# Kernel optimization log

Hardware: AMD Instinct MI355X
Metric: run time of the kernel (lower is better)

Reference implementation:

```python
import jax, jax.numpy as jnp
import numpy as np

DIM = 2048
HEAD = 256
SEQ = 4096

def setup_inputs() -> dict:
    key = jax.random.key(0)
    ks = jax.random.split(key, 7)
    s = 1.0 / np.sqrt(DIM)
    return {
        "marketStateBatch": jax.random.normal(ks[0], (SEQ, DIM), dtype=jnp.float32),
        "Wq": jax.random.uniform(ks[1], (HEAD, DIM), jnp.float32, -s, s),
        "bq": jax.random.uniform(ks[2], (HEAD,), jnp.float32, -s, s),
        "Wk": jax.random.uniform(ks[3], (HEAD, DIM), jnp.float32, -s, s),
        "bk": jax.random.uniform(ks[4], (HEAD,), jnp.float32, -s, s),
        "Wv": jax.random.uniform(ks[5], (HEAD, DIM), jnp.float32, -s, s),
        "bv": jax.random.uniform(ks[6], (HEAD,), jnp.float32, -s, s),
    }

def reference(marketStateBatch, Wq, bq, Wk, bk, Wv, bv):
    x = marketStateBatch  # [S, D]
    q = x @ Wq.T + bq     # [S, H]
    k = x @ Wk.T + bk     # [S, H]
    v = x @ Wv.T + bv     # [S, H]
    # NOTE: original scales by sqrt(dimensionSize), the INPUT dim, not head dim.
    scores = (q @ k.T) * (1.0 / np.sqrt(DIM))  # [S, S]
    S = x.shape[0]
    causal = jnp.tril(jnp.ones((S, S), dtype=bool))
    scores = jnp.where(causal, scores, -jnp.inf)
    attn = jax.nn.softmax(scores, axis=-1)
    # torch.nan_to_num(attn, 0.0): rows are never all -inf here (diag kept),
    # but replicate the op faithfully.
    attn = jnp.nan_to_num(attn, nan=0.0)
    return attn @ v  # [S, H]
```

## Files before the change

### kernel.cpp

```cpp
#include <hip/hip_runtime.h>
#include <stdint.h>

#define SEQ 4096
#define DIMK 2048
#define HD 256

typedef __attribute__((ext_vector_type(8))) short bf16x8;
typedef __attribute__((ext_vector_type(4))) short u16x4;
typedef __attribute__((ext_vector_type(4))) float f32x4;
typedef __attribute__((ext_vector_type(16))) float f32x16;
typedef unsigned short u16;
typedef unsigned int u32;

#define BAR() asm volatile("s_barrier" ::: "memory")
#define VMCNT(n) asm volatile("s_waitcnt vmcnt(" #n ")" ::: "memory")

__device__ __forceinline__ u16 f2bf(float f) {
    u32 u = __float_as_uint(f);
    u += 0x7FFFu + ((u >> 16) & 1u);
    return (u16)(u >> 16);
}

__device__ __forceinline__ float bf2f(u16 h) {
    u32 u = ((u32)h) << 16;
    return __uint_as_float(u);
}

__device__ __forceinline__ bf16x8 pack8(f32x4 a0, f32x4 a1) {
    bf16x8 v8;
    v8[0]=(short)f2bf(a0[0]); v8[1]=(short)f2bf(a0[1]);
    v8[2]=(short)f2bf(a0[2]); v8[3]=(short)f2bf(a0[3]);
    v8[4]=(short)f2bf(a1[0]); v8[5]=(short)f2bf(a1[1]);
    v8[6]=(short)f2bf(a1[2]); v8[7]=(short)f2bf(a1[3]);
    return v8;
}

__device__ __forceinline__ void gl16(const void* g, void* l) {
    __builtin_amdgcn_global_load_lds(
        (const __attribute__((address_space(1))) void*)g,
        (__attribute__((address_space(3))) void*)l, 16, 0, 0);
}

__device__ __forceinline__ u32 cvtpk(float lo, float hi) {
    u32 d;
    asm("v_cvt_pk_bf16_f32 %0, %1, %2" : "=v"(d) : "v"(lo), "v"(hi));
    return d;
}

__device__ __forceinline__ void plswap(u32& x, u32& y) {
#if __has_builtin(__builtin_amdgcn_permlane32_swap)
    typedef int i32x2 __attribute__((ext_vector_type(2)));
    i32x2 r = __builtin_amdgcn_permlane32_swap((int)x, (int)y, false, false);
    x = (u32)r[0]; y = (u32)r[1];
#else
    asm("v_permlane32_swap_b32 %0, %1" : "+v"(x), "+v"(y));
#endif
}

__global__ __launch_bounds__(256) void cvt_all2(
    const float* __restrict__ x, const float* __restrict__ Wq,
    const float* __restrict__ Wk, const float* __restrict__ Wv,
    u16* __restrict__ xb_sw, u16* __restrict__ wb_sw)
{
    const int y = blockIdx.y;
    int i = blockIdx.x * 256 + threadIdx.x;
    int stride = gridDim.x * 256;
    if (y == 0) {
        for (; i < SEQ*DIMK/8; i += stride) {
            int row = i >> 8, c8 = i & 255;
            f32x4 a0 = *(const f32x4*)(x + (size_t)row*DIMK + c8*8);
            f32x4 a1 = *(const f32x4*)(x + (size_t)row*DIMK + c8*8 + 4);
            int mt = row >> 6, rl = row & 63, kt = c8 >> 3, sl = c8 & 7;
            size_t dst = ((size_t)(mt*32 + kt))*4096 + rl*64 + ((sl ^ (rl&7))*8);
            *(bf16x8*)(xb_sw + dst) = pack8(a0, a1);
        }
    } else {
        const float* W = (y==1) ? Wq : (y==2) ? Wk : Wv;
        for (; i < HD*DIMK/8; i += stride) {
            int row = i >> 8, c8 = i & 255;
            f32x4 a0 = *(const f32x4*)(W + (size_t)row*DIMK + c8*8);
            f32x4 a1 = *(const f32x4*)(W + (size_t)row*DIMK + c8*8 + 4);
            int gr = (y-1)*256 + row;
            int nt = gr >> 7, rl = gr & 127, kt = c8 >> 3, sl = c8 & 7;
            size_t dst = ((size_t)(nt*32 + kt))*8192 + rl*64 + ((sl ^ (rl&7))*8);
            *(bf16x8*)(wb_sw + dst) = pack8(a0, a1);
        }
    }
}

__global__ __launch_bounds__(256, 2) void qkv_gemm3(
    const u16* __restrict__ xb_sw, const u16* __restrict__ wb_sw,
    const float* __restrict__ bq, const float* __restrict__ bk,
    const float* __restrict__ bv,
    u16* __restrict__ qb, u16* __restrict__ kb_t, u16* __restrict__ vt_t)
{
    __shared__ char Ab[2][16384];
    __shared__ char Bb[2][16384];

    const int tid = threadIdx.x;
    const int L = tid & 63;
    const int w = tid >> 6;
    const int l31 = L & 31, h = L >> 5;
    const int wr = w >> 1, wc = w & 1;
    const int mt2 = blockIdx.x;
    const int y   = blockIdx.y;
    const int z   = y >> 1;
    const float* bias = (z==0) ? bq : (z==1) ? bk : bv;

    const u16* a0 = xb_sw + ((size_t)((mt2*2 + (w>>1))*32))*4096 + (w&1)*2048 + L*8;
    const u16* b0 = wb_sw + ((size_t)(y*32))*8192 + w*2048 + L*8;

    auto stage = [&](int kt, int b) {
        const u16* ag = a0 + (size_t)kt*4096;
        const u16* bg = b0 + (size_t)kt*8192;
        char* al = Ab[b] + w*4096;
        char* bl = Bb[b] + w*4096;
        #pragma unroll
        for (int i = 0; i < 4; ++i) gl16(ag + i*512, al + i*1024);
        #pragma unroll
        for (int i = 0; i < 4; ++i) gl16(bg + i*512, bl + i*1024);
    };

    stage(0, 0);
    stage(1, 1);

    f32x16 acc[2][2];
    #pragma unroll
    for (int m = 0; m < 2; ++m)
        #pragma unroll
        for (int n = 0; n < 2; ++n)
            #pragma unroll
            for (int e = 0; e < 16; ++e) acc[m][n][e] = 0.f;

    for (int kt = 0; kt < 32; ++kt) {
        if (kt < 31) { VMCNT(8); } else { VMCNT(0); }
        BAR();
        const char* A = Ab[kt & 1];
        const char* B = Bb[kt & 1];
        __builtin_amdgcn_s_setprio(1);
        #pragma unroll
        for (int c = 0; c < 4; ++c) {
            const int sl = 2*c + h;
            bf16x8 af[2], bfr[2];
            #pragma unroll
            for (int m = 0; m < 2; ++m) {
                int row = wr*64 + m*32 + l31;
                af[m] = *(const bf16x8*)(A + (row>>6)*8192 + (row&63)*128
                                           + ((sl ^ (row&7)) << 4));
            }
            #pragma unroll
            for (int n = 0; n < 2; ++n) {
                int brow = wc*64 + n*32 + l31;
                bfr[n] = *(const bf16x8*)(B + brow*128 + ((sl ^ (brow&7)) << 4));
            }
            #pragma unroll
            for (int m = 0; m < 2; ++m)
                #pragma unroll
                for (int n = 0; n < 2; ++n)
                    acc[m][n] = __builtin_amdgcn_mfma_f32_32x32x16_bf16(
                        af[m], bfr[n], acc[m][n], 0, 0, 0);
        }
        __builtin_amdgcn_s_setprio(0);
        BAR();
        if (kt + 2 < 32) stage(kt + 2, kt & 1);
    }

    const int m0 = mt2*128;
    const float qs = 0.03187936f;
    #pragma unroll
    for (int n = 0; n < 2; ++n) {
        const int hc = ((y&1)*128 + wc*64 + n*32 + l31) & 255;
        const float bcol = bias[hc];
        #pragma unroll
        for (int m = 0; m < 2; ++m) {
            const int rbase = m0 + wr*64 + m*32;
            if (z == 0) {
                #pragma unroll
                for (int e = 0; e < 16; ++e) {
                    int grow = rbase + (e&3) + 8*(e>>2) + 4*h;
                    qb[(size_t)grow*HD + hc] = f2bf((acc[m][n][e] + bcol) * qs);
                }
            } else if (z == 1) {
                #pragma unroll
                for (int e = 0; e < 16; ++e) {
                    int grow = rbase + (e&3) + 8*(e>>2) + 4*h;
                    int t = grow >> 5, rl = grow & 31;
                    kb_t[(size_t)t*8192 + rl*256 + (((hc>>3) ^ (rl&7))*8) + (hc&7)]
                        = f2bf(acc[m][n][e] + bcol);
                }
            } else {
                const int t = rbase >> 5;
                #pragma unroll
                for (int e4 = 0; e4 < 4; ++e4) {
                    int kl0 = 8*e4 + 4*h;
                    u16x4 pk;
                    #pragma unroll
                    for (int j = 0; j < 4; ++j)
                        pk[j] = (short)f2bf(acc[m][n][e4*4 + j] + bcol);
                    *(u16x4*)(vt_t + (size_t)t*8192 + hc*32 +
                              ((e4 ^ (hc&3) ^ ((hc>>2)&3))*8) + (kl0&7)) = pk;
                }
            }
        }
    }
}

__global__ __launch_bounds__(256, 2) void attn_part6(
    const u16* __restrict__ qb, const u16* __restrict__ kb_t,
    const u16* __restrict__ vt_t,
    u16* __restrict__ po, float* __restrict__ pm, float* __restrict__ pl,
    int C)
{
    __shared__ char Kb[2][16384];
    __shared__ char Vb[2][16384];

    const int pid = blockIdx.x;
    int Q = 0, a0 = 0;
    for (int k = 0; k < 32; ++k) {
        int nsk = (4*k + 4 + C - 1) / C;
        if (pid < a0 + nsk) { Q = k; break; }
        a0 += nsk;
    }
    const int s  = pid - a0;
    const int nt = 4*Q + 4;
    const int t0 = s*C;
    const int t1 = min(t0 + C, nt);

    const int tid = threadIdx.x;
    const int L = tid & 63;
    const int w = tid >> 6;
    const int l31 = L & 31;
    const int h   = L >> 5;
    const int qg  = Q*128 + w*32 + l31;
    const int vsw = (l31 & 3) ^ ((l31 >> 2) & 3);
    const int kx  = l31 & 7;

    auto stage = [&](int t, int b) {
        const u16* kg = kb_t + (size_t)t*8192 + w*2048 + L*8;
        const u16* vg = vt_t + (size_t)t*8192 + w*2048 + L*8;
        char* kl = Kb[b] + w*4096;
        char* vl = Vb[b] + w*4096;
        #pragma unroll
        for (int i = 0; i < 4; ++i) gl16(kg + i*512, kl + i*1024);
        #pragma unroll
        for (int i = 0; i < 4; ++i) gl16(vg + i*512, vl + i*1024);
    };

    stage(t0, t0 & 1);
    if (t0 + 1 < t1) stage(t0 + 1, (t0 + 1) & 1);
    else             stage(t0,     (t0 + 1) & 1);

    bf16x8 qf[16];
    {
        const u16* qp = qb + (size_t)qg*HD + h*8;
        #pragma unroll
        for (int c = 0; c < 16; ++c) qf[c] = *(const bf16x8*)(qp + c*16);
    }

    f32x16 o[8];
    #pragma unroll
    for (int ht = 0; ht < 8; ++ht)
        #pragma unroll
        for (int e = 0; e < 16; ++e) o[ht][e] = 0.f;
    float mrun = -1e30f, lrun = 0.f;

    for (int t = t0; t < t1; ++t) {
        if (t + 1 < t1) { VMCNT(8); } else { VMCNT(0); }
        BAR();
        const char* K = Kb[t & 1];
        const char* V = Vb[t & 1];

        #define LDK(c) (*(const bf16x8*)(K + l31*512 + (((2*(c) + h) ^ kx) << 4)))
        f32x16 sv;
        #pragma unroll
        for (int e = 0; e < 16; ++e) sv[e] = 0.f;
        __builtin_amdgcn_s_setprio(1);
        {
            bf16x8 ka = LDK(0), kb_ = LDK(1), kc = LDK(2), kd = LDK(3);
            sv = __builtin_amdgcn_mfma_f32_32x32x16_bf16(ka,  qf[0],  sv, 0,0,0); ka  = LDK(4);
            sv = __builtin_amdgcn_mfma_f32_32x32x16_bf16(kb_, qf[1],  sv, 0,0,0); kb_ = LDK(5);
            sv = __builtin_amdgcn_mfma_f32_32x32x16_bf16(kc,  qf[2],  sv, 0,0,0); kc  = LDK(6);
            sv = __builtin_amdgcn_mfma_f32_32x32x16_bf16(kd,  qf[3],  sv, 0,0,0); kd  = LDK(7);
            sv = __builtin_amdgcn_mfma_f32_32x32x16_bf16(ka,  qf[4],  sv, 0,0,0); ka  = LDK(8);
            sv = __builtin_amdgcn_mfma_f32_32x32x16_bf16(kb_, qf[5],  sv, 0,0,0); kb_ = LDK(9);
            sv = __builtin_amdgcn_mfma_f32_32x32x16_bf16(kc,  qf[6],  sv, 0,0,0); kc  = LDK(10);
            sv = __builtin_amdgcn_mfma_f32_32x32x16_bf16(kd,  qf[7],  sv, 0,0,0); kd  = LDK(11);
            sv = __builtin_amdgcn_mfma_f32_32x32x16_bf16(ka,  qf[8],  sv, 0,0,0); ka  = LDK(12);
            sv = __builtin_amdgcn_mfma_f32_32x32x16_bf16(kb_, qf[9],  sv, 0,0,0); kb_ = LDK(13);
            sv = __builtin_amdgcn_mfma_f32_32x32x16_bf16(kc,  qf[10], sv, 0,0,0); kc  = LDK(14);
            sv = __builtin_amdgcn_mfma_f32_32x32x16_bf16(kd,  qf[11], sv, 0,0,0); kd  = LDK(15);
            sv = __builtin_amdgcn_mfma_f32_32x32x16_bf16(ka,  qf[12], sv, 0,0,0);
            sv = __builtin_amdgcn_mfma_f32_32x32x16_bf16(kb_, qf[13], sv, 0,0,0);
            sv = __builtin_amdgcn_mfma_f32_32x32x16_bf16(kc,  qf[14], sv, 0,0,0);
            sv = __builtin_amdgcn_mfma_f32_32x32x16_bf16(kd,  qf[15], sv, 0,0,0);
        }
        #undef LDK
        __builtin_amdgcn_s_setprio(0);

        if (t*32 + 31 > Q*128 + w*32) {
            #pragma unroll
            for (int e = 0; e < 16; ++e) {
                int kvr = (e & 3) + 8*(e >> 2) + 4*h;
                if (t*32 + kvr > qg) sv[e] = -__builtin_inff();
            }
        }

        float m0_ = fmaxf(fmaxf(sv[0],sv[1]),  fmaxf(sv[2],sv[3]));
        float m1_ = fmaxf(fmaxf(sv[4],sv[5]),  fmaxf(sv[6],sv[7]));
        float m2_ = fmaxf(fmaxf(sv[8],sv[9]),  fmaxf(sv[10],sv[11]));
        float m3_ = fmaxf(fmaxf(sv[12],sv[13]),fmaxf(sv[14],sv[15]));
        float mx = fmaxf(fmaxf(m0_,m1_), fmaxf(m2_,m3_));
        mx = fmaxf(mx, __shfl_xor(mx, 32));
        if (__any(mx > mrun + 8.0f)) {
            float mnew  = fmaxf(mrun, mx);
            float alpha = exp2f(mrun - mnew);
            lrun *= alpha;
            #pragma unroll
            for (int ht = 0; ht < 8; ++ht) o[ht] *= alpha;
            mrun = mnew;
        }
        #pragma unroll
        for (int e = 0; e < 16; ++e) sv[e] = exp2f(sv[e] - mrun);
        float r0 = ((sv[0]+sv[1])+(sv[2]+sv[3])) + ((sv[4]+sv[5])+(sv[6]+sv[7]));
        float r1 = ((sv[8]+sv[9])+(sv[10]+sv[11])) + ((sv[12]+sv[13])+(sv[14]+sv[15]));
        float rs = r0 + r1;
        rs += __shfl_xor(rs, 32);
        lrun += rs;

        union { u32 wd[4]; bf16x8 v8; } up0, up1;
        {
            u32 A = cvtpk(sv[0],  sv[1]),  B = cvtpk(sv[2],  sv[3]);
            u32 Cc= cvtpk(sv[4],  sv[5]),  D = cvtpk(sv[6],  sv[7]);
            plswap(A, Cc); plswap(B, D);
            up0.wd[0]=A; up0.wd[1]=B; up0.wd[2]=Cc; up0.wd[3]=D;
            u32 A1 = cvtpk(sv[8],  sv[9]),  B1 = cvtpk(sv[10], sv[11]);
            u32 C1 = cvtpk(sv[12], sv[13]), D1 = cvtpk(sv[14], sv[15]);
            plswap(A1, C1); plswap(B1, D1);
            up1.wd[0]=A1; up1.wd[1]=B1; up1.wd[2]=C1; up1.wd[3]=D1;
        }
        bf16x8 pa0 = up0.v8, pa1 = up1.v8;

        __builtin_amdgcn_s_setprio(1);
        #pragma unroll
        for (int ht = 0; ht < 8; ++ht) {
            const char* vrow = V + (ht*32 + l31)*64;
            bf16x8 vf0 = *(const bf16x8*)(vrow + (((h)     ^ vsw) << 4));
            bf16x8 vf1 = *(const bf16x8*)(vrow + (((2 + h) ^ vsw) << 4));
            o[ht] = __builtin_amdgcn_mfma_f32_32x32x16_bf16(vf0, pa0, o[ht], 0, 0, 0);
            o[ht] = __builtin_amdgcn_mfma_f32_32x32x16_bf16(vf1, pa1, o[ht], 0, 0, 0);
        }
        __builtin_amdgcn_s_setprio(0);

        BAR();
        stage(min(t + 2, t1 - 1), t & 1);
    }

    VMCNT(0);

    if (h == 0) {
        pm[(size_t)pid*128 + w*32 + l31] = mrun;
        pl[(size_t)pid*128 + w*32 + l31] = lrun;
    }
    u16* op = po + ((size_t)pid*128 + w*32 + l31) * 256;
    #pragma unroll
    for (int ht = 0; ht < 8; ++ht)
        #pragma unroll
        for (int j = 0; j < 8; ++j) {
            u32 pk = (u32)f2bf(o[ht][2*j]) | ((u32)f2bf(o[ht][2*j+1]) << 16);
            int hdb = ht*32 + (j & 1)*2 + (j >> 1)*8 + 4*h;
            *(u32*)(op + hdb) = pk;
        }
}

__global__ __launch_bounds__(256) void attn_combine5(
    const u16* __restrict__ po, const float* __restrict__ pm,
    const float* __restrict__ pl, float* __restrict__ out, int C)
{
    const int tid = threadIdx.x;
    const int row = blockIdx.x * 16 + (tid >> 4);
    const int cg  = tid & 15;
    const int Q   = row >> 7, rr = row & 127;
    const int nt  = 4*Q + 4;
    const int ns  = (nt + C - 1) / C;
    int pid0 = 0;
    for (int k = 0; k < Q; ++k) pid0 += (4*k + 4 + C - 1) / C;

    float M = -1e30f;
    for (int s = 0; s < ns; ++s)
        M = fmaxf(M, pm[(size_t)(pid0+s)*128 + rr]);

    float lt = 0.f;
    f32x4 acc[4];
    f32x4 zero = {0.f,0.f,0.f,0.f};
    #pragma unroll
    for (int v = 0; v < 4; ++v) acc[v] = zero;

    for (int s = 0; s < ns; ++s) {
        float ms  = pm[(size_t)(pid0+s)*128 + rr];
        float wgt = exp2f(ms - M);
        lt += wgt * pl[(size_t)(pid0+s)*128 + rr];
        const u16* p = po + ((size_t)(pid0+s)*128 + rr)*256 + cg*16;
        #pragma unroll
        for (int v = 0; v < 4; ++v) {
            u16x4 pv = *(const u16x4*)(p + v*4);
            #pragma unroll
            for (int e = 0; e < 4; ++e)
                acc[v][e] += wgt * bf2f((u16)pv[e]);
        }
    }
    float inv = 1.f / lt;
    f32x4* op = (f32x4*)(out + (size_t)row*256 + cg*16);
    #pragma unroll
    for (int v = 0; v < 4; ++v) op[v] = acc[v] * inv;
}

extern "C" void kernel_launch(void* const* d_in, const int* in_sizes, int n_in,
                              void* d_out, int out_size, void* d_ws, size_t ws_size,
                              hipStream_t stream) {
    const float* x  = (const float*)d_in[0];
    const float* Wq = (const float*)d_in[1];
    const float* bq = (const float*)d_in[2];
    const float* Wk = (const float*)d_in[3];
    const float* bk = (const float*)d_in[4];
    const float* Wv = (const float*)d_in[5];
    const float* bv = (const float*)d_in[6];
    float* out = (float*)d_out;

    const size_t xb_bytes  = (size_t)SEQ * DIMK * 2;
    const size_t wb_bytes  = (size_t)768 * DIMK * 2;
    const size_t qkv_bytes = (size_t)SEQ * HD * 2;
    const size_t base = xb_bytes + wb_bytes + 3*qkv_bytes;

    int C = 64;
    size_t npid = 0;
    const int cand[4] = {5, 8, 16, 64};
    for (int ci = 0; ci < 4; ++ci) {
        int c = cand[ci];
        size_t np = 0;
        for (int k = 0; k < 32; ++k) np += (size_t)(4*k + 4 + c - 1) / c;
        size_t need = base + np * ((size_t)128*256*2 + 2*128*4);
        if (need <= ws_size) { C = c; npid = np; break; }
        if (ci == 3) { C = c; npid = np; }
    }

    char* p = (char*)d_ws;
    u16* xb_sw = (u16*)p; p += xb_bytes;
    u16* wb_sw = (u16*)p; p += wb_bytes;
    u16* qbuf  = (u16*)p; p += qkv_bytes;
    u16* kb_t  = (u16*)p; p += qkv_bytes;
    u16* vt_t  = (u16*)p; p += qkv_bytes;
    u16* po    = (u16*)p; p += npid * 128 * 256 * 2;
    float* pm  = (float*)p; p += npid * 128 * 4;
    float* pl  = (float*)p; p += npid * 128 * 4;

    cvt_all2<<<dim3(512, 4), 256, 0, stream>>>(x, Wq, Wk, Wv, xb_sw, wb_sw);

    qkv_gemm3<<<dim3(SEQ/128, 6), 256, 0, stream>>>(
        xb_sw, wb_sw, bq, bk, bv, qbuf, kb_t, vt_t);

    attn_part6<<<(int)npid, 256, 0, stream>>>(
        qbuf, kb_t, vt_t, po, pm, pl, C);

    attn_combine5<<<SEQ/16, 256, 0, stream>>>(po, pm, pl, out, C);
}
```

Before: 93.06 us.

## Halve QKV GEMM N-tile to 64 columns and double grid for occupancy

After: 88.56 us. 1.05x faster.

```diff
diff --git a/kernel.cpp b/kernel.cpp
--- a/kernel.cpp
+++ b/kernel.cpp
@@ -88,14 +88,14 @@
     }
 }
 
-__global__ __launch_bounds__(256, 2) void qkv_gemm3(
+__global__ __launch_bounds__(256, 3) void qkv_gemm4(
     const u16* __restrict__ xb_sw, const u16* __restrict__ wb_sw,
     const float* __restrict__ bq, const float* __restrict__ bk,
     const float* __restrict__ bv,
     u16* __restrict__ qb, u16* __restrict__ kb_t, u16* __restrict__ vt_t)
 {
     __shared__ char Ab[2][16384];
-    __shared__ char Bb[2][16384];
+    __shared__ char Bb[2][8192];
 
     const int tid = threadIdx.x;
     const int L = tid & 63;
@@ -104,36 +104,34 @@
     const int wr = w >> 1, wc = w & 1;
     const int mt2 = blockIdx.x;
     const int y   = blockIdx.y;
-    const int z   = y >> 1;
+    const int z   = y >> 2;
     const float* bias = (z==0) ? bq : (z==1) ? bk : bv;
 
     const u16* a0 = xb_sw + ((size_t)((mt2*2 + (w>>1))*32))*4096 + (w&1)*2048 + L*8;
-    const u16* b0 = wb_sw + ((size_t)(y*32))*8192 + w*2048 + L*8;
+    const u16* b0 = wb_sw + ((size_t)((y>>1)*32))*8192 + (y&1)*4096 + w*1024 + L*8;
 
     auto stage = [&](int kt, int b) {
         const u16* ag = a0 + (size_t)kt*4096;
         const u16* bg = b0 + (size_t)kt*8192;
         char* al = Ab[b] + w*4096;
-        char* bl = Bb[b] + w*4096;
+        char* bl = Bb[b] + w*2048;
         #pragma unroll
         for (int i = 0; i < 4; ++i) gl16(ag + i*512, al + i*1024);
-        #pragma unroll
-        for (int i = 0; i < 4; ++i) gl16(bg + i*512, bl + i*1024);
+        gl16(bg,       bl);
+        gl16(bg + 512, bl + 1024);
     };
 
     stage(0, 0);
     stage(1, 1);
 
-    f32x16 acc[2][2];
+    f32x16 acc[2];
     #pragma unroll
     for (int m = 0; m < 2; ++m)
         #pragma unroll
-        for (int n = 0; n < 2; ++n)
-            #pragma unroll
-            for (int e = 0; e < 16; ++e) acc[m][n][e] = 0.f;
+        for (int e = 0; e < 16; ++e) acc[m][e] = 0.f;
 
     for (int kt = 0; kt < 32; ++kt) {
-        if (kt < 31) { VMCNT(8); } else { VMCNT(0); }
+        if (kt < 31) { VMCNT(6); } else { VMCNT(0); }
         BAR();
         const char* A = Ab[kt & 1];
         const char* B = Bb[kt & 1];
@@ -141,24 +139,18 @@
         #pragma unroll
         for (int c = 0; c < 4; ++c) {
             const int sl = 2*c + h;
-            bf16x8 af[2], bfr[2];
+            const int brow = wc*32 + l31;
+            bf16x8 bfr = *(const bf16x8*)(B + brow*128 + ((sl ^ (brow&7)) << 4));
+            bf16x8 af[2];
             #pragma unroll
             for (int m = 0; m < 2; ++m) {
-                int row = wr*64 + m*32 + l31;
-                af[m] = *(const bf16x8*)(A + (row>>6)*8192 + (row&63)*128
-                                           + ((sl ^ (row&7)) << 4));
+                int rlo = m*32 + l31;
+                af[m] = *(const bf16x8*)(A + wr*8192 + rlo*128 + ((sl ^ (rlo&7)) << 4));
             }
             #pragma unroll
-            for (int n = 0; n < 2; ++n) {
-                int brow = wc*64 + n*32 + l31;
-                bfr[n] = *(const bf16x8*)(B + brow*128 + ((sl ^ (brow&7)) << 4));
-            }
-            #pragma unroll
             for (int m = 0; m < 2; ++m)
-                #pragma unroll
-                for (int n = 0; n < 2; ++n)
-                    acc[m][n] = __builtin_amdgcn_mfma_f32_32x32x16_bf16(
-                        af[m], bfr[n], acc[m][n], 0, 0, 0);
+                acc[m] = __builtin_amdgcn_mfma_f32_32x32x16_bf16(
+                    af[m], bfr, acc[m], 0, 0, 0);
         }
         __builtin_amdgcn_s_setprio(0);
         BAR();
@@ -167,39 +159,36 @@
 
     const int m0 = mt2*128;
     const float qs = 0.03187936f;
-    #pragma unroll
-    for (int n = 0; n < 2; ++n) {
-        const int hc = ((y&1)*128 + wc*64 + n*32 + l31) & 255;
-        const float bcol = bias[hc];
-        #pragma unroll
-        for (int m = 0; m < 2; ++m) {
-            const int rbase = m0 + wr*64 + m*32;
-            if (z == 0) {
+    const int hc = (y & 3)*64 + wc*32 + l31;
+    const float bcol = bias[hc];
+    #pragma unroll
+    for (int m = 0; m < 2; ++m) {
+        const int rbase = m0 + wr*64 + m*32;
+        if (z == 0) {
+            #pragma unroll
+            for (int e = 0; e < 16; ++e) {
+                int grow = rbase + (e&3) + 8*(e>>2) + 4*h;
+                qb[(size_t)grow*HD + hc] = f2bf((acc[m][e] + bcol) * qs);
+            }
+        } else if (z == 1) {
+            #pragma unroll
+            for (int e = 0; e < 16; ++e) {
+                int grow = rbase + (e&3) + 8*(e>>2) + 4*h;
+                int t = grow >> 5, rl = grow & 31;
+                kb_t[(size_t)t*8192 + rl*256 + (((hc>>3) ^ (rl&7))*8) + (hc&7)]
+                    = f2bf(acc[m][e] + bcol);
+            }
+        } else {
+            const int t = rbase >> 5;
+            #pragma unroll
+            for (int e4 = 0; e4 < 4; ++e4) {
+                int kl0 = 8*e4 + 4*h;
+                u16x4 pk;
                 #pragma unroll
-                for (int e = 0; e < 16; ++e) {
-                    int grow = rbase + (e&3) + 8*(e>>2) + 4*h;
-                    qb[(size_t)grow*HD + hc] = f2bf((acc[m][n][e] + bcol) * qs);
-                }
-            } else if (z == 1) {
-                #pragma unroll
-                for (int e = 0; e < 16; ++e) {
-                    int grow = rbase + (e&3) + 8*(e>>2) + 4*h;
-                    int t = grow >> 5, rl = grow & 31;
-                    kb_t[(size_t)t*8192 + rl*256 + (((hc>>3) ^ (rl&7))*8) + (hc&7)]
-                        = f2bf(acc[m][n][e] + bcol);
-                }
-            } else {
-                const int t = rbase >> 5;
-                #pragma unroll
-                for (int e4 = 0; e4 < 4; ++e4) {
-                    int kl0 = 8*e4 + 4*h;
-                    u16x4 pk;
-                    #pragma unroll
-                    for (int j = 0; j < 4; ++j)
-                        pk[j] = (short)f2bf(acc[m][n][e4*4 + j] + bcol);
-                    *(u16x4*)(vt_t + (size_t)t*8192 + hc*32 +
-                              ((e4 ^ (hc&3) ^ ((hc>>2)&3))*8) + (kl0&7)) = pk;
-                }
+                for (int j = 0; j < 4; ++j)
+                    pk[j] = (short)f2bf(acc[m][e4*4 + j] + bcol);
+                *(u16x4*)(vt_t + (size_t)t*8192 + hc*32 +
+                          ((e4 ^ (hc&3) ^ ((hc>>2)&3))*8) + (kl0&7)) = pk;
             }
         }
     }
@@ -455,7 +444,7 @@
 
     cvt_all2<<<dim3(512, 4), 256, 0, stream>>>(x, Wq, Wk, Wv, xb_sw, wb_sw);
 
-    qkv_gemm3<<<dim3(SEQ/128, 6), 256, 0, stream>>>(
+    qkv_gemm4<<<dim3(SEQ/128, 12), 256, 0, stream>>>(
         xb_sw, wb_sw, bq, bk, bv, qbuf, kb_t, vt_t);
 
     attn_part6<<<(int)npid, 256, 0, stream>>>(
```
